# Optimization experiments

Hardware: AMD Instinct MI355X
Metric: run time of the kernel (lower is better)

## Reference

```python
import jax, jax.numpy as jnp
import numpy as np

N_NODES = 100000
N_EDGES = 1600000
N_GRAPHS = 1024
DIM_IN = 128
DIM_SF = 32
DIM_OUT = 8
EPS = 1e-5


def setup_inputs() -> dict:
    key = jax.random.key(0)
    ks = jax.random.split(key, 16)
    feat = jax.random.normal(ks[0], (N_NODES, DIM_IN), dtype=jnp.float32)
    self_feat = jax.random.normal(ks[1], (N_GRAPHS, DIM_SF), dtype=jnp.float32)
    src = jax.random.randint(ks[2], (N_EDGES,), 0, N_NODES)
    dst = jax.random.randint(ks[3], (N_EDGES,), 0, N_NODES)
    node2graph = jnp.sort(jax.random.randint(ks[4], (N_NODES,), 0, N_GRAPHS))

    def lin(k, din, dout):
        s = 1.0 / np.sqrt(din)
        kw, kb = jax.random.split(k)
        W = jax.random.uniform(kw, (din, dout), minval=-s, maxval=s, dtype=jnp.float32)
        b = jax.random.uniform(kb, (dout,), minval=-s, maxval=s, dtype=jnp.float32)
        return W, b

    W1, b1 = lin(ks[5], DIM_IN, 100)
    W2, b2 = lin(ks[6], 100, 20)
    Wf1, bf1 = lin(ks[7], 20 * DIM_SF, 128)
    Wf2, bf2 = lin(ks[8], 128, 32)
    Wf3, bf3 = lin(ks[9], 32, DIM_OUT)
    g1 = jnp.ones((128,), jnp.float32); be1 = jnp.zeros((128,), jnp.float32)
    g2 = jnp.ones((32,), jnp.float32); be2 = jnp.zeros((32,), jnp.float32)
    return dict(feat=feat, self_feat=self_feat, src=src, dst=dst,
                node2graph=node2graph, W1=W1, b1=b1, W2=W2, b2=b2,
                Wf1=Wf1, bf1=bf1, g1=g1, be1=be1,
                Wf2=Wf2, bf2=bf2, g2=g2, be2=be2, Wf3=Wf3, bf3=bf3)


def _gcn_layer(h, src, dst, W, b):
    # copy_u + mean reduce: segment-mean of source features onto destinations.
    n = h.shape[0]
    msum = jax.ops.segment_sum(h[src], dst, num_segments=n)        # [N, d]
    deg = jax.ops.segment_sum(jnp.ones((src.shape[0], 1), h.dtype), dst,
                              num_segments=n)                      # [N, 1]
    # DGL: nodes with no incoming messages keep their previous 'h'.
    agg = jnp.where(deg > 0, msum / jnp.maximum(deg, 1.0), h)
    return agg @ W + b


def _bn(x, gamma, beta):
    # BatchNorm1d in training mode: biased batch statistics.
    mu = jnp.mean(x, axis=0)
    var = jnp.mean((x - mu) ** 2, axis=0)
    return (x - mu) / jnp.sqrt(var + EPS) * gamma + beta


def reference(feat, self_feat, src, dst, node2graph,
              W1, b1, W2, b2, Wf1, bf1, g1, be1, Wf2, bf2, g2, be2, Wf3, bf3):
    h = jax.nn.relu(_gcn_layer(feat, src, dst, W1, b1))            # [N, 100]
    h = jax.nn.relu(_gcn_layer(h, src, dst, W2, b2))               # [N, 20]
    # dgl.mean_nodes: per-graph mean pooling
    hsum = jax.ops.segment_sum(h, node2graph, num_segments=N_GRAPHS)
    cnt = jax.ops.segment_sum(jnp.ones((h.shape[0], 1), h.dtype), node2graph,
                              num_segments=N_GRAPHS)
    hg = hsum / jnp.maximum(cnt, 1.0)                              # [G, 20]
    # Kronecker fusion: bmm(hg[:, :, None], self_feat[:, None, :])
    fused = (hg[:, :, None] * self_feat[:, None, :]).reshape(hg.shape[0], -1)
    out = jax.nn.relu(_bn(fused @ Wf1 + bf1, g1, be1))
    out = jax.nn.relu(_bn(out @ Wf2 + bf2, g2, be2))
    return out @ Wf3 + bf3                                         # [G, 8]
```

## Files before the change

kernel.cpp:

```cpp
#include <hip/hip_runtime.h>
#include <hip/hip_fp16.h>

#define N_NODES 100000
#define N_EDGES 1600000
#define N_GRAPHS 1024
#define DIM_IN 128
#define D1 100
#define D1P 128
#define D2 20
#define D2P 32
#define DIM_SF 32
#define DF1 128
#define DF2 32
#define DOUT 8
#define EPS 1e-5f
#define NPW 8

typedef _Float16 hh2 __attribute__((ext_vector_type(2)));

__device__ __forceinline__ void fdacc(unsigned u, float& lo, float& hi) {
  const hh2 MLO = {(_Float16)1.0f, (_Float16)0.0f};
  const hh2 MHI = {(_Float16)0.0f, (_Float16)1.0f};
  hh2 h = __builtin_bit_cast(hh2, u);
  lo = __builtin_amdgcn_fdot2(h, MLO, lo, false);
  hi = __builtin_amdgcn_fdot2(h, MHI, hi, false);
}

__device__ __forceinline__ unsigned pkadd(unsigned a, unsigned b) {
  __half2 x = __builtin_bit_cast(__half2, a);
  __half2 y = __builtin_bit_cast(__half2, b);
  return __builtin_bit_cast(unsigned, __hadd2(x, y));
}

#define NBK 512
#define BW 196
#define EPB 4096
#define NBLK1 ((N_EDGES + EPB - 1) / EPB)

__global__ void __launch_bounds__(256) k_bscatter(const int* __restrict__ src,
                                                  const int* __restrict__ dst,
                                                  int* __restrict__ bucket_cnt,
                                                  unsigned* __restrict__ packed_out) {
  __shared__ int hist[NBK];
  __shared__ int lbase[NBK];
  __shared__ int gbase[NBK];
  __shared__ int ssum[256];
  __shared__ unsigned sval[EPB];
  __shared__ int spos[EPB];
  int t = threadIdx.x, blk = blockIdx.x;
  for (int i = t; i < NBK; i += 256) hist[i] = 0;
  __syncthreads();
  int base = blk * EPB;
  unsigned pk[16]; int bn[16]; int rk[16];
#pragma unroll
  for (int r = 0; r < 16; r++) {
    int e = base + r * 256 + t;
    bn[r] = -1;
    if (e < N_EDGES) {
      int dv = dst[e];
      unsigned b = (unsigned)dv / BW;
      unsigned ld = (unsigned)dv - b * BW;
      bn[r] = (int)b;
      pk[r] = ((unsigned)src[e] << 8) | ld;
      rk[r] = atomicAdd(&hist[b], 1);
    }
  }
  __syncthreads();
  int h0 = hist[2 * t], h1 = hist[2 * t + 1];
  int s = h0 + h1;
  ssum[t] = s; __syncthreads();
  for (int off = 1; off < 256; off <<= 1) {
    int x = (t >= off) ? ssum[t - off] : 0;
    __syncthreads();
    ssum[t] += x;
    __syncthreads();
  }
  int excl = ssum[t] - s;
  lbase[2 * t] = excl;
  lbase[2 * t + 1] = excl + h0;
  gbase[2 * t]     = (h0 > 0) ? (2 * t) * EPB     + atomicAdd(&bucket_cnt[2 * t],     h0) : 0;
  gbase[2 * t + 1] = (h1 > 0) ? (2 * t + 1) * EPB + atomicAdd(&bucket_cnt[2 * t + 1], h1) : 0;
  __syncthreads();
#pragma unroll
  for (int r = 0; r < 16; r++) {
    if (bn[r] >= 0) {
      int li = lbase[bn[r]] + rk[r];
      sval[li] = pk[r];
      spos[li] = gbase[bn[r]] + rk[r];
    }
  }
  __syncthreads();
  int cnt = N_EDGES - base; if (cnt > EPB) cnt = EPB;
  for (int i = t; i < cnt; i += 256) packed_out[spos[i]] = sval[i];
}

__global__ void __launch_bounds__(256) k_bfine(const unsigned* __restrict__ packed_in,
                                               const int* __restrict__ bucket_cnt,
                                               int* __restrict__ csr,
                                               int* __restrict__ deg,
                                               int* __restrict__ row_off) {
  __shared__ unsigned sval[EPB];
  __shared__ int scsr[EPB];
  __shared__ int hist[256];
  __shared__ int soff[256];
  __shared__ int cur[256];
  int b = blockIdx.x, t = threadIdx.x;
  int start = b * EPB;
  int cnt = bucket_cnt[b];
  if (cnt > EPB) cnt = EPB;
  hist[t] = 0;
  __syncthreads();
  for (int i = t; i < cnt; i += 256) {
    unsigned v = packed_in[start + i];
    sval[i] = v;
    atomicAdd(&hist[v & 255u], 1);
  }
  __syncthreads();
  int h = hist[t];
  soff[t] = h; __syncthreads();
  for (int off = 1; off < 256; off <<= 1) {
    int x = (t >= off) ? soff[t - off] : 0;
    __syncthreads();
    soff[t] += x;
    __syncthreads();
  }
  int excl = soff[t] - h;
  cur[t] = excl;
  int n = b * BW + t;
  if (t < BW && n < N_NODES) { deg[n] = h; row_off[n] = start + excl; }
  __syncthreads();
  for (int i = t; i < cnt; i += 256) {
    unsigned v = sval[i];
    int pos = atomicAdd(&cur[v & 255u], 1);
    scsr[pos] = (int)(v >> 8);
  }
  __syncthreads();
  for (int i = t; i < cnt; i += 256) csr[start + i] = scsr[i];
}

__global__ void __launch_bounds__(256) k_goff(const int* __restrict__ n2g,
                                              int* __restrict__ g_off) {
  int g = blockIdx.x * 256 + threadIdx.x;
  if (g > N_GRAPHS) return;
  if (g == N_GRAPHS) { g_off[g] = N_NODES; return; }
  int lo = 0, hi = N_NODES;
  while (lo < hi) {
    int mid = (lo + hi) >> 1;
    if (n2g[mid] < g) lo = mid + 1; else hi = mid;
  }
  g_off[g] = lo;
}

__global__ void __launch_bounds__(256) k_gemm1(const float* __restrict__ feat,
                                               const float* __restrict__ W1,
                                               __half* __restrict__ p1h) {
  __shared__ float w1s[DIM_IN * D1];
  int t = threadIdx.x;
  for (int i = t; i < DIM_IN * D1; i += 256) w1s[i] = W1[i];
  __syncthreads();
  if (t >= 250) return;
  int q = t % 25, ng = t / 25;
  int n0 = blockIdx.x * 80 + ng * 8;
  int c0 = q * 4;
  float acc[8][4] = {{0.f}};
  const float* f0 = feat + (size_t)n0 * DIM_IN;
  for (int k = 0; k < DIM_IN; k += 4) {
    float4 w0 = *(const float4*)&w1s[(k + 0) * D1 + c0];
    float4 w1 = *(const float4*)&w1s[(k + 1) * D1 + c0];
    float4 w2 = *(const float4*)&w1s[(k + 2) * D1 + c0];
    float4 w3 = *(const float4*)&w1s[(k + 3) * D1 + c0];
#pragma unroll
    for (int j = 0; j < 8; j++) {
      float4 f = *(const float4*)(f0 + j * DIM_IN + k);
      acc[j][0] += f.x * w0.x + f.y * w1.x + f.z * w2.x + f.w * w3.x;
      acc[j][1] += f.x * w0.y + f.y * w1.y + f.z * w2.y + f.w * w3.y;
      acc[j][2] += f.x * w0.z + f.y * w1.z + f.z * w2.z + f.w * w3.z;
      acc[j][3] += f.x * w0.w + f.y * w1.w + f.z * w2.w + f.w * w3.w;
    }
  }
#pragma unroll
  for (int j = 0; j < 8; j++) {
    __half2* d2 = (__half2*)(p1h + (size_t)(n0 + j) * D1P + c0);
    d2[0] = __floats2half2_rn(acc[j][0], acc[j][1]);
    d2[1] = __floats2half2_rn(acc[j][2], acc[j][3]);
  }
}

__device__ __forceinline__ void acc8d(uint4 r, float4& A, float4& B) {
  fdacc(r.x, A.x, A.y);
  fdacc(r.y, A.z, A.w);
  fdacc(r.z, B.x, B.y);
  fdacc(r.w, B.z, B.w);
}

__global__ void __launch_bounds__(256) k_agg1(const __half* __restrict__ p1h,
                                              const int* __restrict__ deg,
                                              const int* __restrict__ row_off,
                                              const int* __restrict__ csr,
                                              const float* __restrict__ b1,
                                              const float* __restrict__ W2,
                                              __half* __restrict__ p2h) {
  __shared__ float w2s[D1 * D2];
  __shared__ float b1s[D1];
  __shared__ float hbuf[4][104];
  int t = threadIdx.x;
  for (int i = t; i < D1 * D2; i += 256) w2s[i] = W2[i];
  if (t < D1) b1s[t] = b1[t];
  __syncthreads();
  int w = t >> 6, lane = t & 63;
  int g = lane >> 4, o = lane & 15;
  const size_t oh = (size_t)(o * 8);
  int p = lane / 20;
  int j20 = lane - p * 20;
  int cbeg = (p == 0) ? 0 : (p == 1) ? 33 : 66;
  int cend = (p == 0) ? 33 : (p == 1) ? 66 : 100;
  if (p >= 3) { cbeg = 0; cend = 0; }
  int n0 = (blockIdx.x * 4 + w) * NPW;
  for (int nn = 0; nn < NPW; nn++) {
    int n = n0 + nn;
    int d = deg[n], ro = row_off[n];
    float4 A = {0.f, 0.f, 0.f, 0.f}, B = {0.f, 0.f, 0.f, 0.f};
    if (d > 0) {
      for (int base = 0; base < d; base += 64) {
        int m = d - base; if (m > 64) m = 64;
        int sv = (lane < m) ? csr[ro + base + lane] : 0;
        int nr = m >> 2;
        int r = 0;
        for (; r + 3 < nr; r += 4) {
          int sA = __shfl(sv, r * 4 + g);
          int sB = __shfl(sv, r * 4 + 4 + g);
          int sC = __shfl(sv, r * 4 + 8 + g);
          int sD = __shfl(sv, r * 4 + 12 + g);
          uint4 ra = *(const uint4*)(p1h + (size_t)sA * D1P + oh);
          uint4 rb = *(const uint4*)(p1h + (size_t)sB * D1P + oh);
          uint4 rc = *(const uint4*)(p1h + (size_t)sC * D1P + oh);
          uint4 rd = *(const uint4*)(p1h + (size_t)sD * D1P + oh);
          uint4 u, v2;
          u.x = pkadd(ra.x, rb.x); u.y = pkadd(ra.y, rb.y);
          u.z = pkadd(ra.z, rb.z); u.w = pkadd(ra.w, rb.w);
          v2.x = pkadd(rc.x, rd.x); v2.y = pkadd(rc.y, rd.y);
          v2.z = pkadd(rc.z, rd.z); v2.w = pkadd(rc.w, rd.w);
          acc8d(u, A, B);
          acc8d(v2, A, B);
        }
        if (r + 1 < nr) {
          int sA = __shfl(sv, r * 4 + g);
          int sB = __shfl(sv, r * 4 + 4 + g);
          uint4 ra = *(const uint4*)(p1h + (size_t)sA * D1P + oh);
          uint4 rb = *(const uint4*)(p1h + (size_t)sB * D1P + oh);
          uint4 u;
          u.x = pkadd(ra.x, rb.x); u.y = pkadd(ra.y, rb.y);
          u.z = pkadd(ra.z, rb.z); u.w = pkadd(ra.w, rb.w);
          acc8d(u, A, B);
          r += 2;
        }
        if (r < nr) {
          int sA = __shfl(sv, r * 4 + g);
          uint4 ra = *(const uint4*)(p1h + (size_t)sA * D1P + oh);
          acc8d(ra, A, B);
        }
        int rem = m & 3;
        int sT = __shfl(sv, nr * 4 + g);
        if (rem && g < rem) {
          uint4 ra = *(const uint4*)(p1h + (size_t)sT * D1P + oh);
          acc8d(ra, A, B);
        }
      }
    } else {
      if (g == 0) {
        uint4 ra = *(const uint4*)(p1h + (size_t)n * D1P + oh);
        acc8d(ra, A, B);
      }
    }
    float v[8] = {A.x, A.y, A.z, A.w, B.x, B.y, B.z, B.w};
#pragma unroll
    for (int j = 0; j < 8; j++) {
      v[j] += __shfl_down(v[j], 32);
      v[j] += __shfl_down(v[j], 16);
    }
    if (lane < 13) {
      float inv = (d > 0) ? 1.0f / (float)d : 1.0f;
#pragma unroll
      for (int j = 0; j < 8; j++) {
        int ch = 8 * lane + j;
        if (ch < D1) hbuf[w][ch] = fmaxf(v[j] * inv + b1s[ch], 0.f);
      }
    }
    float acc = 0.f;
    for (int c = cbeg; c < cend; c++) acc += hbuf[w][c] * w2s[c * D2 + j20];
    float t1 = __shfl_down(acc, 20);
    float t2 = __shfl_down(acc, 40);
    acc += t1 + t2;
    if (lane < D2)       p2h[(size_t)n * D2P + lane] = __float2half_rn(acc);
    else if (lane < D2P) p2h[(size_t)n * D2P + lane] = __float2half_rn(0.f);
  }
}

__global__ void __launch_bounds__(512) k_agg2(const __half* __restrict__ p2h,
                                              const int* __restrict__ deg,
                                              const int* __restrict__ row_off,
                                              const int* __restrict__ csr,
                                              const float* __restrict__ b2,
                                              const int* __restrict__ g_off,
                                              float* __restrict__ hg) {
  __shared__ float ssum[D2];
  __shared__ float b2s[D2];
  int g = blockIdx.x, t = threadIdx.x;
  if (t < D2) { ssum[t] = 0.f; b2s[t] = b2[t]; }
  __syncthreads();
  const unsigned* pu = (const unsigned*)p2h;
  int n_lo = g_off[g], n_hi = g_off[g + 1];
  int nn = n_hi - n_lo;
  if (t < 510) {
    int nid = t / 5, c2 = t - (t / 5) * 5;
    int ch = 4 * c2;
    for (int ni = nid; ni < nn; ni += 102) {
      int n = n_lo + ni;
      int d = deg[n], ro = row_off[n];
      float v0, v1, v2, v3;
      if (d > 0) {
        float a0 = 0.f, a1 = 0.f, a2 = 0.f, a3 = 0.f;
        float b0 = 0.f, b1 = 0.f, bb2 = 0.f, b3 = 0.f;
        int e = 0;
        for (; e + 3 < d; e += 4) {
          int s0 = csr[ro + e],     s1 = csr[ro + e + 1];
          int s2 = csr[ro + e + 2], s3 = csr[ro + e + 3];
          uint2 r0 = *(const uint2*)(pu + (size_t)s0 * 16 + 2 * c2);
          uint2 r1 = *(const uint2*)(pu + (size_t)s1 * 16 + 2 * c2);
          uint2 r2 = *(const uint2*)(pu + (size_t)s2 * 16 + 2 * c2);
          uint2 r3 = *(const uint2*)(pu + (size_t)s3 * 16 + 2 * c2);
          fdacc(r0.x, a0, a1); fdacc(r0.y, a2, a3);
          fdacc(r1.x, b0, b1); fdacc(r1.y, bb2, b3);
          fdacc(r2.x, a0, a1); fdacc(r2.y, a2, a3);
          fdacc(r3.x, b0, b1); fdacc(r3.y, bb2, b3);
        }
        for (; e < d; e++) {
          int s0 = csr[ro + e];
          uint2 r0 = *(const uint2*)(pu + (size_t)s0 * 16 + 2 * c2);
          fdacc(r0.x, a0, a1); fdacc(r0.y, a2, a3);
        }
        float inv = 1.0f / (float)d;
        v0 = (a0 + b0) * inv; v1 = (a1 + b1) * inv;
        v2 = (a2 + bb2) * inv; v3 = (a3 + b3) * inv;
      } else {
        uint2 r0 = *(const uint2*)(pu + (size_t)n * 16 + 2 * c2);
        v0 = v1 = v2 = v3 = 0.f;
        fdacc(r0.x, v0, v1); fdacc(r0.y, v2, v3);
      }
      atomicAdd(&ssum[ch + 0], fmaxf(v0 + b2s[ch + 0], 0.f));
      atomicAdd(&ssum[ch + 1], fmaxf(v1 + b2s[ch + 1], 0.f));
      atomicAdd(&ssum[ch + 2], fmaxf(v2 + b2s[ch + 2], 0.f));
      atomicAdd(&ssum[ch + 3], fmaxf(v3 + b2s[ch + 3], 0.f));
    }
  }
  __syncthreads();
  if (t < D2) {
    float inv = (nn > 0) ? 1.0f / (float)nn : 0.f;
    hg[g * D2 + t] = ssum[t] * inv;
  }
}

__global__ void __launch_bounds__(128) k_mlp1(const float* __restrict__ hg,
                                              const float* __restrict__ sf,
                                              const float* __restrict__ Wf1,
                                              const float* __restrict__ bf1,
                                              float* __restrict__ y1) {
  __shared__ float prod[D2 * DIM_SF];
  __shared__ float hgl[D2], sfl[DIM_SF];
  int g = blockIdx.x, t = threadIdx.x;
  if (t < D2) hgl[t] = hg[g * D2 + t];
  if (t < DIM_SF) sfl[t] = sf[g * DIM_SF + t];
  __syncthreads();
  for (int i = t; i < D2 * DIM_SF; i += 128) prod[i] = hgl[i >> 5] * sfl[i & 31];
  __syncthreads();
  float acc = bf1[t];
#pragma unroll 4
  for (int k = 0; k < D2 * DIM_SF; k++) acc += prod[k] * Wf1[k * DF1 + t];
  y1[g * DF1 + t] = acc;
}

__global__ void k_bnstats(const float* __restrict__ x, int ld,
                          float* __restrict__ mu, float* __restrict__ rstd) {
  __shared__ float ssum[256], ssq[256];
  int c = blockIdx.x, t = threadIdx.x;
  float s = 0.f, q = 0.f;
  for (int r = t; r < N_GRAPHS; r += 256) { float v = x[r * ld + c]; s += v; q += v * v; }
  ssum[t] = s; ssq[t] = q; __syncthreads();
  for (int off = 128; off > 0; off >>= 1) {
    if (t < off) { ssum[t] += ssum[t + off]; ssq[t] += ssq[t + off]; }
    __syncthreads();
  }
  if (t == 0) {
    float m = ssum[0] / (float)N_GRAPHS;
    float var = ssq[0] / (float)N_GRAPHS - m * m;
    mu[c] = m;
    rstd[c] = rsqrtf(var + EPS);
  }
}

__global__ void k_mlp2(const float* __restrict__ y1, const float* __restrict__ mu1,
                       const float* __restrict__ rstd1, const float* __restrict__ g1,
                       const float* __restrict__ be1, const float* __restrict__ Wf2,
                       const float* __restrict__ bf2, float* __restrict__ y2) {
  int idx = blockIdx.x * 256 + threadIdx.x;
  int g = idx >> 5, o = idx & 31;
  float acc = bf2[o];
  for (int k = 0; k < DF1; k++) {
    float x = (y1[g * DF1 + k] - mu1[k]) * rstd1[k] * g1[k] + be1[k];
    x = fmaxf(x, 0.f);
    acc += x * Wf2[k * DF2 + o];
  }
  y2[g * DF2 + o] = acc;
}

__global__ void k_mlp3(const float* __restrict__ y2, const float* __restrict__ mu2,
                       const float* __restrict__ rstd2, const float* __restrict__ g2,
                       const float* __restrict__ be2, const float* __restrict__ Wf3,
                       const float* __restrict__ bf3, float* __restrict__ out) {
  int idx = blockIdx.x * 256 + threadIdx.x;
  int g = idx >> 3, o = idx & 7;
  float acc = bf3[o];
  for (int k = 0; k < DF2; k++) {
    float x = (y2[g * DF2 + k] - mu2[k]) * rstd2[k] * g2[k] + be2[k];
    x = fmaxf(x, 0.f);
    acc += x * Wf3[k * DOUT + o];
  }
  out[g * DOUT + o] = acc;
}

extern "C" void kernel_launch(void* const* d_in, const int* in_sizes, int n_in,
                              void* d_out, int out_size, void* d_ws, size_t ws_size,
                              hipStream_t stream) {
  const float* feat = (const float*)d_in[0];
  const float* sf   = (const float*)d_in[1];
  const int*   src  = (const int*)d_in[2];
  const int*   dst  = (const int*)d_in[3];
  const int*   n2g  = (const int*)d_in[4];
  const float* W1   = (const float*)d_in[5];
  const float* b1   = (const float*)d_in[6];
  const float* W2   = (const float*)d_in[7];
  const float* b2   = (const float*)d_in[8];
  const float* Wf1  = (const float*)d_in[9];
  const float* bf1  = (const float*)d_in[10];
  const float* g1   = (const float*)d_in[11];
  const float* be1  = (const float*)d_in[12];
  const float* Wf2  = (const float*)d_in[13];
  const float* bf2  = (const float*)d_in[14];
  const float* g2   = (const float*)d_in[15];
  const float* be2  = (const float*)d_in[16];
  const float* Wf3  = (const float*)d_in[17];
  const float* bf3  = (const float*)d_in[18];
  float* out = (float*)d_out;

  char* ws = (char*)d_ws;
  size_t off = 0;
  auto alloc = [&](size_t bytes) -> void* {
    void* p = ws + off;
    off = (off + bytes + 255) & ~(size_t)255;
    return p;
  };
  int*      bucket_cnt = (int*)alloc(NBK * 4);
  size_t zero_bytes = off;
  int*      g_offs   = (int*)alloc((N_GRAPHS + 1) * 4);
  float*    hg       = (float*)alloc(N_GRAPHS * D2 * 4);
  int*      deg      = (int*)alloc(N_NODES * 4);
  int*      row_off  = (int*)alloc(N_NODES * 4);
  unsigned* packed   = (unsigned*)alloc((size_t)NBK * EPB * 4);
  int*      csr      = (int*)alloc((size_t)NBK * EPB * 4);
  __half*   p1h      = (__half*)alloc((size_t)N_NODES * D1P * 2);
  __half*   p2h      = (__half*)alloc((size_t)N_NODES * D2P * 2);
  float*    y1       = (float*)alloc((size_t)N_GRAPHS * DF1 * 4);
  float*    y2       = (float*)alloc((size_t)N_GRAPHS * DF2 * 4);
  float*    mu1      = (float*)alloc(DF1 * 4);
  float*    rstd1    = (float*)alloc(DF1 * 4);
  float*    mu2      = (float*)alloc(DF2 * 4);
  float*    rstd2    = (float*)alloc(DF2 * 4);

  hipMemsetAsync(d_ws, 0, zero_bytes, stream);

  k_goff<<<(N_GRAPHS + 1 + 255) / 256, 256, 0, stream>>>(n2g, g_offs);
  k_bscatter<<<NBLK1, 256, 0, stream>>>(src, dst, bucket_cnt, packed);
  k_bfine<<<NBK, 256, 0, stream>>>(packed, bucket_cnt, csr, deg, row_off);
  k_gemm1<<<N_NODES / 80, 256, 0, stream>>>(feat, W1, p1h);
  k_agg1<<<N_NODES / (4 * NPW), 256, 0, stream>>>(p1h, deg, row_off, csr, b1, W2, p2h);
  k_agg2<<<N_GRAPHS, 512, 0, stream>>>(p2h, deg, row_off, csr, b2, g_offs, hg);
  k_mlp1<<<N_GRAPHS, 128, 0, stream>>>(hg, sf, Wf1, bf1, y1);
  k_bnstats<<<DF1, 256, 0, stream>>>(y1, DF1, mu1, rstd1);
  k_mlp2<<<(N_GRAPHS * DF2) / 256, 256, 0, stream>>>(y1, mu1, rstd1, g1, be1, Wf2, bf2, y2);
  k_bnstats<<<DF2, 256, 0, stream>>>(y2, DF2, mu2, rstd2);
  k_mlp3<<<(N_GRAPHS * DOUT) / 256, 256, 0, stream>>>(y2, mu2, rstd2, g2, be2, Wf3, bf3, out);
}
```

Measured before the change: 410.9 us.

## Merge edge bucketing with first GEMM, drop memset, rework graph-pool aggregation

Edge bucket scatter and the feat@W1 GEMM now run as one launch. Separate block ranges take each role and share the same shared-memory buffer, so the two independent stages overlap. The memset of bucket counters moves into the graph-offset kernel, which saves a separate launch. The layer-2 aggregation/pooling kernel now gives one wavefront per node. Edges are cooperatively loaded 64 at a time and spread via shuffles, 16 edges in parallel with 4 lanes per row. Results are reduced with shuffles and accumulated per graph in registers before a few shared atomics, in place of per-node atomics. The fused kernel's shared-memory footprint is the GEMM's 51 KB for every block, which may reduce occupancy for the scatter blocks.

```diff
diff --git a/kernel.cpp b/kernel.cpp
--- a/kernel.cpp
+++ b/kernel.cpp
@@ -36,62 +36,115 @@
 #define BW 196
 #define EPB 4096
 #define NBLK1 ((N_EDGES + EPB - 1) / EPB)
-
-__global__ void __launch_bounds__(256) k_bscatter(const int* __restrict__ src,
-                                                  const int* __restrict__ dst,
-                                                  int* __restrict__ bucket_cnt,
-                                                  unsigned* __restrict__ packed_out) {
-  __shared__ int hist[NBK];
-  __shared__ int lbase[NBK];
-  __shared__ int gbase[NBK];
-  __shared__ int ssum[256];
-  __shared__ unsigned sval[EPB];
-  __shared__ int spos[EPB];
-  int t = threadIdx.x, blk = blockIdx.x;
-  for (int i = t; i < NBK; i += 256) hist[i] = 0;
-  __syncthreads();
-  int base = blk * EPB;
-  unsigned pk[16]; int bn[16]; int rk[16];
-#pragma unroll
-  for (int r = 0; r < 16; r++) {
-    int e = base + r * 256 + t;
-    bn[r] = -1;
-    if (e < N_EDGES) {
-      int dv = dst[e];
-      unsigned b = (unsigned)dv / BW;
-      unsigned ld = (unsigned)dv - b * BW;
-      bn[r] = (int)b;
-      pk[r] = ((unsigned)src[e] << 8) | ld;
-      rk[r] = atomicAdd(&hist[b], 1);
-    }
-  }
-  __syncthreads();
-  int h0 = hist[2 * t], h1 = hist[2 * t + 1];
-  int s = h0 + h1;
-  ssum[t] = s; __syncthreads();
-  for (int off = 1; off < 256; off <<= 1) {
-    int x = (t >= off) ? ssum[t - off] : 0;
-    __syncthreads();
-    ssum[t] += x;
-    __syncthreads();
-  }
-  int excl = ssum[t] - s;
-  lbase[2 * t] = excl;
-  lbase[2 * t + 1] = excl + h0;
-  gbase[2 * t]     = (h0 > 0) ? (2 * t) * EPB     + atomicAdd(&bucket_cnt[2 * t],     h0) : 0;
-  gbase[2 * t + 1] = (h1 > 0) ? (2 * t + 1) * EPB + atomicAdd(&bucket_cnt[2 * t + 1], h1) : 0;
-  __syncthreads();
-#pragma unroll
-  for (int r = 0; r < 16; r++) {
-    if (bn[r] >= 0) {
-      int li = lbase[bn[r]] + rk[r];
-      sval[li] = pk[r];
-      spos[li] = gbase[bn[r]] + rk[r];
-    }
-  }
-  __syncthreads();
-  int cnt = N_EDGES - base; if (cnt > EPB) cnt = EPB;
-  for (int i = t; i < cnt; i += 256) packed_out[spos[i]] = sval[i];
+#define GEMM1_NB (N_NODES / 80)
+
+__global__ void __launch_bounds__(256) k_goff(const int* __restrict__ n2g,
+                                              int* __restrict__ g_off,
+                                              int* __restrict__ bucket_cnt) {
+  int g = blockIdx.x * 256 + threadIdx.x;
+  if (g < NBK) bucket_cnt[g] = 0;
+  if (g > N_GRAPHS) return;
+  if (g == N_GRAPHS) { g_off[g] = N_NODES; return; }
+  int lo = 0, hi = N_NODES;
+  while (lo < hi) {
+    int mid = (lo + hi) >> 1;
+    if (n2g[mid] < g) lo = mid + 1; else hi = mid;
+  }
+  g_off[g] = lo;
+}
+
+__global__ void __launch_bounds__(256) k_sc_gemm(const int* __restrict__ src,
+                                                 const int* __restrict__ dst,
+                                                 int* __restrict__ bucket_cnt,
+                                                 unsigned* __restrict__ packed_out,
+                                                 const float* __restrict__ feat,
+                                                 const float* __restrict__ W1,
+                                                 __half* __restrict__ p1h) {
+  __shared__ __align__(16) char smem[DIM_IN * D1 * 4];
+  int t = threadIdx.x;
+  if (blockIdx.x < NBLK1) {
+    int* hist   = (int*)smem;
+    int* lbase  = (int*)(smem + 2048);
+    int* gbase  = (int*)(smem + 4096);
+    int* ssum   = (int*)(smem + 6144);
+    unsigned* sval = (unsigned*)(smem + 7168);
+    int* spos   = (int*)(smem + 23552);
+    int blk = blockIdx.x;
+    for (int i = t; i < NBK; i += 256) hist[i] = 0;
+    __syncthreads();
+    int base = blk * EPB;
+    unsigned pk[16]; int bn[16]; int rk[16];
+#pragma unroll
+    for (int r = 0; r < 16; r++) {
+      int e = base + r * 256 + t;
+      bn[r] = -1;
+      if (e < N_EDGES) {
+        int dv = dst[e];
+        unsigned b = (unsigned)dv / BW;
+        unsigned ld = (unsigned)dv - b * BW;
+        bn[r] = (int)b;
+        pk[r] = ((unsigned)src[e] << 8) | ld;
+        rk[r] = atomicAdd(&hist[b], 1);
+      }
+    }
+    __syncthreads();
+    int h0 = hist[2 * t], h1 = hist[2 * t + 1];
+    int s = h0 + h1;
+    ssum[t] = s; __syncthreads();
+    for (int off = 1; off < 256; off <<= 1) {
+      int x = (t >= off) ? ssum[t - off] : 0;
+      __syncthreads();
+      ssum[t] += x;
+      __syncthreads();
+    }
+    int excl = ssum[t] - s;
+    lbase[2 * t] = excl;
+    lbase[2 * t + 1] = excl + h0;
+    gbase[2 * t]     = (h0 > 0) ? (2 * t) * EPB     + atomicAdd(&bucket_cnt[2 * t],     h0) : 0;
+    gbase[2 * t + 1] = (h1 > 0) ? (2 * t + 1) * EPB + atomicAdd(&bucket_cnt[2 * t + 1], h1) : 0;
+    __syncthreads();
+#pragma unroll
+    for (int r = 0; r < 16; r++) {
+      if (bn[r] >= 0) {
+        int li = lbase[bn[r]] + rk[r];
+        sval[li] = pk[r];
+        spos[li] = gbase[bn[r]] + rk[r];
+      }
+    }
+    __syncthreads();
+    int cnt = N_EDGES - base; if (cnt > EPB) cnt = EPB;
+    for (int i = t; i < cnt; i += 256) packed_out[spos[i]] = sval[i];
+  } else {
+    float* w1s = (float*)smem;
+    for (int i = t; i < DIM_IN * D1; i += 256) w1s[i] = W1[i];
+    __syncthreads();
+    if (t >= 250) return;
+    int q = t % 25, ng = t / 25;
+    int n0 = (int)(blockIdx.x - NBLK1) * 80 + ng * 8;
+    int c0 = q * 4;
+    float acc[8][4] = {{0.f}};
+    const float* f0 = feat + (size_t)n0 * DIM_IN;
+    for (int k = 0; k < DIM_IN; k += 4) {
+      float4 w0 = *(const float4*)&w1s[(k + 0) * D1 + c0];
+      float4 w1 = *(const float4*)&w1s[(k + 1) * D1 + c0];
+      float4 w2 = *(const float4*)&w1s[(k + 2) * D1 + c0];
+      float4 w3 = *(const float4*)&w1s[(k + 3) * D1 + c0];
+#pragma unroll
+      for (int j = 0; j < 8; j++) {
+        float4 f = *(const float4*)(f0 + j * DIM_IN + k);
+        acc[j][0] += f.x * w0.x + f.y * w1.x + f.z * w2.x + f.w * w3.x;
+        acc[j][1] += f.x * w0.y + f.y * w1.y + f.z * w2.y + f.w * w3.y;
+        acc[j][2] += f.x * w0.z + f.y * w1.z + f.z * w2.z + f.w * w3.z;
+        acc[j][3] += f.x * w0.w + f.y * w1.w + f.z * w2.w + f.w * w3.w;
+      }
+    }
+#pragma unroll
+    for (int j = 0; j < 8; j++) {
+      __half2* d2 = (__half2*)(p1h + (size_t)(n0 + j) * D1P + c0);
+      d2[0] = __floats2half2_rn(acc[j][0], acc[j][1]);
+      d2[1] = __floats2half2_rn(acc[j][2], acc[j][3]);
+    }
+  }
 }
 
 __global__ void __launch_bounds__(256) k_bfine(const unsigned* __restrict__ packed_in,
@@ -136,54 +189,6 @@
   }
   __syncthreads();
   for (int i = t; i < cnt; i += 256) csr[start + i] = scsr[i];
-}
-
-__global__ void __launch_bounds__(256) k_goff(const int* __restrict__ n2g,
-                                              int* __restrict__ g_off) {
-  int g = blockIdx.x * 256 + threadIdx.x;
-  if (g > N_GRAPHS) return;
-  if (g == N_GRAPHS) { g_off[g] = N_NODES; return; }
-  int lo = 0, hi = N_NODES;
-  while (lo < hi) {
-    int mid = (lo + hi) >> 1;
-    if (n2g[mid] < g) lo = mid + 1; else hi = mid;
-  }
-  g_off[g] = lo;
-}
-
-__global__ void __launch_bounds__(256) k_gemm1(const float* __restrict__ feat,
-                                               const float* __restrict__ W1,
-                                               __half* __restrict__ p1h) {
-  __shared__ float w1s[DIM_IN * D1];
-  int t = threadIdx.x;
-  for (int i = t; i < DIM_IN * D1; i += 256) w1s[i] = W1[i];
-  __syncthreads();
-  if (t >= 250) return;
-  int q = t % 25, ng = t / 25;
-  int n0 = blockIdx.x * 80 + ng * 8;
-  int c0 = q * 4;
-  float acc[8][4] = {{0.f}};
-  const float* f0 = feat + (size_t)n0 * DIM_IN;
-  for (int k = 0; k < DIM_IN; k += 4) {
-    float4 w0 = *(const float4*)&w1s[(k + 0) * D1 + c0];
-    float4 w1 = *(const float4*)&w1s[(k + 1) * D1 + c0];
-    float4 w2 = *(const float4*)&w1s[(k + 2) * D1 + c0];
-    float4 w3 = *(const float4*)&w1s[(k + 3) * D1 + c0];
-#pragma unroll
-    for (int j = 0; j < 8; j++) {
-      float4 f = *(const float4*)(f0 + j * DIM_IN + k);
-      acc[j][0] += f.x * w0.x + f.y * w1.x + f.z * w2.x + f.w * w3.x;
-      acc[j][1] += f.x * w0.y + f.y * w1.y + f.z * w2.y + f.w * w3.y;
-      acc[j][2] += f.x * w0.z + f.y * w1.z + f.z * w2.z + f.w * w3.z;
-      acc[j][3] += f.x * w0.w + f.y * w1.w + f.z * w2.w + f.w * w3.w;
-    }
-  }
-#pragma unroll
-  for (int j = 0; j < 8; j++) {
-    __half2* d2 = (__half2*)(p1h + (size_t)(n0 + j) * D1P + c0);
-    d2[0] = __floats2half2_rn(acc[j][0], acc[j][1]);
-    d2[1] = __floats2half2_rn(acc[j][2], acc[j][3]);
-  }
 }
 
 __device__ __forceinline__ void acc8d(uint4 r, float4& A, float4& B) {
@@ -305,52 +310,88 @@
                                               float* __restrict__ hg) {
   __shared__ float ssum[D2];
   __shared__ float b2s[D2];
-  int g = blockIdx.x, t = threadIdx.x;
+  int t = threadIdx.x, w = t >> 6, lane = t & 63;
+  int g = blockIdx.x;
   if (t < D2) { ssum[t] = 0.f; b2s[t] = b2[t]; }
   __syncthreads();
   const unsigned* pu = (const unsigned*)p2h;
   int n_lo = g_off[g], n_hi = g_off[g + 1];
   int nn = n_hi - n_lo;
-  if (t < 510) {
-    int nid = t / 5, c2 = t - (t / 5) * 5;
-    int ch = 4 * c2;
-    for (int ni = nid; ni < nn; ni += 102) {
-      int n = n_lo + ni;
-      int d = deg[n], ro = row_off[n];
-      float v0, v1, v2, v3;
-      if (d > 0) {
-        float a0 = 0.f, a1 = 0.f, a2 = 0.f, a3 = 0.f;
-        float b0 = 0.f, b1 = 0.f, bb2 = 0.f, b3 = 0.f;
-        int e = 0;
-        for (; e + 3 < d; e += 4) {
-          int s0 = csr[ro + e],     s1 = csr[ro + e + 1];
-          int s2 = csr[ro + e + 2], s3 = csr[ro + e + 3];
-          uint2 r0 = *(const uint2*)(pu + (size_t)s0 * 16 + 2 * c2);
-          uint2 r1 = *(const uint2*)(pu + (size_t)s1 * 16 + 2 * c2);
-          uint2 r2 = *(const uint2*)(pu + (size_t)s2 * 16 + 2 * c2);
-          uint2 r3 = *(const uint2*)(pu + (size_t)s3 * 16 + 2 * c2);
-          fdacc(r0.x, a0, a1); fdacc(r0.y, a2, a3);
-          fdacc(r1.x, b0, b1); fdacc(r1.y, bb2, b3);
-          fdacc(r2.x, a0, a1); fdacc(r2.y, a2, a3);
-          fdacc(r3.x, b0, b1); fdacc(r3.y, bb2, b3);
+  int e16 = lane >> 2, o = lane & 3;
+  bool xtra = (o == 0);
+  float4 GA = {0.f, 0.f, 0.f, 0.f};
+  float4 GX = {0.f, 0.f, 0.f, 0.f};
+  for (int n = n_lo + w; n < n_hi; n += 8) {
+    int d = deg[n], ro = row_off[n];
+    float4 A = {0.f, 0.f, 0.f, 0.f};
+    float4 X = {0.f, 0.f, 0.f, 0.f};
+    if (d > 0) {
+      for (int base = 0; base < d; base += 64) {
+        int m = d - base; if (m > 64) m = 64;
+        int sv = (lane < m) ? csr[ro + base + lane] : 0;
+        int nr = (m + 15) >> 4;
+        for (int r = 0; r < nr; r++) {
+          int ei = r * 16 + e16;
+          int s0 = __shfl(sv, ei);
+          if (ei < m) {
+            const unsigned* row = pu + (size_t)s0 * 16;
+            uint2 ra = *(const uint2*)(row + 2 * o);
+            fdacc(ra.x, A.x, A.y);
+            fdacc(ra.y, A.z, A.w);
+            if (xtra) {
+              uint2 rx = *(const uint2*)(row + 8);
+              fdacc(rx.x, X.x, X.y);
+              fdacc(rx.y, X.z, X.w);
+            }
+          }
         }
-        for (; e < d; e++) {
-          int s0 = csr[ro + e];
-          uint2 r0 = *(const uint2*)(pu + (size_t)s0 * 16 + 2 * c2);
-          fdacc(r0.x, a0, a1); fdacc(r0.y, a2, a3);
+      }
+    } else {
+      if (e16 == 0) {
+        const unsigned* row = pu + (size_t)n * 16;
+        uint2 ra = *(const uint2*)(row + 2 * o);
+        fdacc(ra.x, A.x, A.y);
+        fdacc(ra.y, A.z, A.w);
+        if (xtra) {
+          uint2 rx = *(const uint2*)(row + 8);
+          fdacc(rx.x, X.x, X.y);
+          fdacc(rx.y, X.z, X.w);
         }
-        float inv = 1.0f / (float)d;
-        v0 = (a0 + b0) * inv; v1 = (a1 + b1) * inv;
-        v2 = (a2 + bb2) * inv; v3 = (a3 + b3) * inv;
-      } else {
-        uint2 r0 = *(const uint2*)(pu + (size_t)n * 16 + 2 * c2);
-        v0 = v1 = v2 = v3 = 0.f;
-        fdacc(r0.x, v0, v1); fdacc(r0.y, v2, v3);
-      }
-      atomicAdd(&ssum[ch + 0], fmaxf(v0 + b2s[ch + 0], 0.f));
-      atomicAdd(&ssum[ch + 1], fmaxf(v1 + b2s[ch + 1], 0.f));
-      atomicAdd(&ssum[ch + 2], fmaxf(v2 + b2s[ch + 2], 0.f));
-      atomicAdd(&ssum[ch + 3], fmaxf(v3 + b2s[ch + 3], 0.f));
+      }
+    }
+#pragma unroll
+    for (int sft = 32; sft >= 4; sft >>= 1) {
+      A.x += __shfl_down(A.x, sft); A.y += __shfl_down(A.y, sft);
+      A.z += __shfl_down(A.z, sft); A.w += __shfl_down(A.w, sft);
+      X.x += __shfl_down(X.x, sft); X.y += __shfl_down(X.y, sft);
+      X.z += __shfl_down(X.z, sft); X.w += __shfl_down(X.w, sft);
+    }
+    float inv = (d > 0) ? 1.0f / (float)d : 1.0f;
+    if (lane < 4) {
+      int ch = 4 * lane;
+      GA.x += fmaxf(A.x * inv + b2s[ch + 0], 0.f);
+      GA.y += fmaxf(A.y * inv + b2s[ch + 1], 0.f);
+      GA.z += fmaxf(A.z * inv + b2s[ch + 2], 0.f);
+      GA.w += fmaxf(A.w * inv + b2s[ch + 3], 0.f);
+      if (lane == 0) {
+        GX.x += fmaxf(X.x * inv + b2s[16], 0.f);
+        GX.y += fmaxf(X.y * inv + b2s[17], 0.f);
+        GX.z += fmaxf(X.z * inv + b2s[18], 0.f);
+        GX.w += fmaxf(X.w * inv + b2s[19], 0.f);
+      }
+    }
+  }
+  if (lane < 4) {
+    int ch = 4 * lane;
+    atomicAdd(&ssum[ch + 0], GA.x);
+    atomicAdd(&ssum[ch + 1], GA.y);
+    atomicAdd(&ssum[ch + 2], GA.z);
+    atomicAdd(&ssum[ch + 3], GA.w);
+    if (lane == 0) {
+      atomicAdd(&ssum[16], GX.x);
+      atomicAdd(&ssum[17], GX.y);
+      atomicAdd(&ssum[18], GX.z);
+      atomicAdd(&ssum[19], GX.w);
     }
   }
   __syncthreads();
@@ -460,7 +501,6 @@
     return p;
   };
   int*      bucket_cnt = (int*)alloc(NBK * 4);
-  size_t zero_bytes = off;
   int*      g_offs   = (int*)alloc((N_GRAPHS + 1) * 4);
   float*    hg       = (float*)alloc(N_GRAPHS * D2 * 4);
   int*      deg      = (int*)alloc(N_NODES * 4);
@@ -476,12 +516,10 @@
   float*    mu2      = (float*)alloc(DF2 * 4);
   float*    rstd2    = (float*)alloc(DF2 * 4);
 
-  hipMemsetAsync(d_ws, 0, zero_bytes, stream);
-
-  k_goff<<<(N_GRAPHS + 1 + 255) / 256, 256, 0, stream>>>(n2g, g_offs);
-  k_bscatter<<<NBLK1, 256, 0, stream>>>(src, dst, bucket_cnt, packed);
+  k_goff<<<(N_GRAPHS + 1 + 255) / 256, 256, 0, stream>>>(n2g, g_offs, bucket_cnt);
+  k_sc_gemm<<<NBLK1 + GEMM1_NB, 256, 0, stream>>>(src, dst, bucket_cnt, packed,
+                                                  feat, W1, p1h);
   k_bfine<<<NBK, 256, 0, stream>>>(packed, bucket_cnt, csr, deg, row_off);
-  k_gemm1<<<N_NODES / 80, 256, 0, stream>>>(feat, W1, p1h);
   k_agg1<<<N_NODES / (4 * NPW), 256, 0, stream>>>(p1h, deg, row_off, csr, b1, W2, p2h);
   k_agg2<<<N_GRAPHS, 512, 0, stream>>>(p2h, deg, row_off, csr, b2, g_offs, hg);
   k_mlp1<<<N_GRAPHS, 128, 0, stream>>>(hg, sf, Wf1, bf1, y1);
```

Result: no change. 403.6 us (-1.8%).
